# Performance work log

Measured on AMD Instinct MI355X. Metric: run time of the kernel, lower is better.

## Reference

```python
import jax, jax.numpy as jnp
import numpy as np

B, T, D = 16, 4096, 256
CODEBOOK_SIZE = 1024
COMMITMENT = 1.0


def setup_inputs() -> dict:
    key = jax.random.key(0)
    kx, kc = jax.random.split(key)
    x = jax.random.normal(kx, (B, T, D), dtype=jnp.float32)
    codebook = jax.random.normal(kc, (CODEBOOK_SIZE, D), dtype=jnp.float32)
    return {"x": x, "codebook": codebook}


def reference(x, codebook):
    # x: [B, T, D] continuous latents; codebook: [K, D]
    flat = x.reshape(-1, x.shape[-1])  # [N, D]
    # does not affect argmin but is kept for faithfulness to torch.cdist-style math)
    x_sq = jnp.sum(flat * flat, axis=1, keepdims=True)            # [N, 1]
    c_sq = jnp.sum(codebook * codebook, axis=1)                   # [K]
    dist = x_sq - 2.0 * (flat @ codebook.T) + c_sq[None, :]       # [N, K]
    indices = jnp.argmin(dist, axis=1)                            # [N] int
    quantized = codebook[indices].reshape(x.shape)                # gather, [B, T, D]
    # commitment loss: encoder pulled toward (stopped) codes
    commit_loss = COMMITMENT * jnp.mean(
        (x - jax.lax.stop_gradient(quantized)) ** 2
    )
    # straight-through estimator
    out = x + jax.lax.stop_gradient(quantized - x)
    return out, indices.reshape(x.shape[:-1]), commit_loss
```

## Files before the change

kernel.cpp:

```cpp
#include <hip/hip_runtime.h>

#define N_TOK 65536
#define DIM   256
#define KCODE 1024

#define NTHREADS 256
#define TM 128
#define TN 128
#define BK 32
#define NCHUNK 8
#define NSTAGE 24
#define OTM 128

#define REFINE_EPS 0.125f
#define TIE_THETA 1.0e-4

#define WS_CSQ_OFF   16
#define WS_IDX_OFF   2048
#define WS_PAIRS_OFF (WS_IDX_OFF + N_TOK)
#define WS_CBPK_OFF  (WS_PAIRS_OFF + N_TOK * NCHUNK * 4)

typedef float f32x4  __attribute__((ext_vector_type(4)));
typedef short bf16x8 __attribute__((ext_vector_type(8)));
typedef short s16x8  __attribute__((ext_vector_type(8)));

__global__ void rowsq_np_kernel(const float* __restrict__ m,
                                float* __restrict__ out,
                                float* __restrict__ loss_ws, int rows) {
#pragma clang fp contract(off)
    if (blockIdx.x == 0 && threadIdx.x == 0) loss_ws[0] = 0.0f;
    int row = blockIdx.x * 16 + (threadIdx.x >> 4);
    int l   = threadIdx.x & 15;
    if (row >= rows) return;
    int h = l >> 3;
    int j = l & 7;
    const float* p = m + (size_t)row * DIM + h * 128 + j;
    float v = p[0];
    float r = v * v;
#pragma unroll
    for (int i = 1; i < 16; ++i) {
        float w  = p[i * 8];
        float w2 = w * w;
        r = r + w2;
    }
    float t = r + __shfl_xor(r, 1);
    t = t + __shfl_xor(t, 2);
    t = t + __shfl_xor(t, 4);
    t = t + __shfl_xor(t, 8);
    if (l == 0) out[row] = t;
}

__device__ __forceinline__ void ins2(float d, int idx,
                                     float& d1, int& i1, float& d2, int& i2) {
    if (d < d1 || (d == d1 && idx < i1)) {
        d2 = d1; i2 = i1; d1 = d; i1 = idx;
    } else if ((d < d2 || (d == d2 && idx < i2)) && idx != i1) {
        d2 = d; i2 = idx;
    }
}

__device__ __forceinline__ void f2bf_split(float v, short& hi, short& lo) {
    unsigned u = __float_as_uint(v);
    unsigned r = (u + 0x7fffu + ((u >> 16) & 1u)) >> 16;
    hi = (short)r;
    float hf = __uint_as_float(r << 16);
    float lf = v - hf;
    unsigned u2 = __float_as_uint(lf);
    unsigned r2 = (u2 + 0x7fffu + ((u2 >> 16) & 1u)) >> 16;
    lo = (short)r2;
}

__global__ void pack_tiles_kernel(const float* __restrict__ src,
                                  unsigned short* __restrict__ dst,
                                  int total, int swz) {
    int tid = blockIdx.x * blockDim.x + threadIdx.x;
    if (tid >= total) return;
    int s   = tid & 3;
    int r   = (tid >> 2) & 127;
    int kc  = (tid >> 9) & 7;
    int g   = tid >> 12;
    int oct = swz ? (s ^ ((r >> 1) & 3)) : s;

    const float4* xr = reinterpret_cast<const float4*>(
        src + ((size_t)(g * 128 + r)) * DIM + kc * 32 + oct * 8);
    float4 v0 = xr[0];
    float4 v1 = xr[1];

    float f[8] = {v0.x, v0.y, v0.z, v0.w, v1.x, v1.y, v1.z, v1.w};
    s16x8 hv, lv;
#pragma unroll
    for (int i = 0; i < 8; ++i) {
        short h, l;
        f2bf_split(f[i], h, l);
        hv[i] = h; lv[i] = l;
    }
    size_t base_hi = (((size_t)(g * 16 + kc) * 128 + r) << 5) + s * 8;
    size_t base_lo = (((size_t)(g * 16 + 8 + kc) * 128 + r) << 5) + s * 8;
    *reinterpret_cast<s16x8*>(dst + base_hi) = hv;
    *reinterpret_cast<s16x8*>(dst + base_lo) = lv;
}

__device__ __forceinline__ void gload_lds16(const unsigned short* g, unsigned short* lds) {
    __builtin_amdgcn_global_load_lds(
        (const __attribute__((address_space(1))) unsigned int*)g,
        (__attribute__((address_space(3))) unsigned int*)lds, 16, 0, 0);
}

__launch_bounds__(NTHREADS, 4)
__global__ void vq_main_kernel(const unsigned short* __restrict__ xpk,
                               const unsigned short* __restrict__ cbpk,
                               const float* __restrict__ csq,
                               float4* __restrict__ pairs) {
    __shared__ __align__(16) unsigned short shbuf[2][TM * BK];
    __shared__ float4 pairs_sh[TM][2];

    const int tid  = threadIdx.x;
    const int w    = tid >> 6;
    const int wy   = w >> 1;
    const int wx   = w & 1;
    const int lane = tid & 63;
    const int lm   = lane & 15;
    const int q    = lane >> 4;

    const int bx     = blockIdx.x;
    const int jj     = bx >> 3;
    const int grp    = (bx & 7) + ((jj >> 3) << 3);
    const int cchunk = jj & 7;
    const int tok0   = grp * TM;
    const int code0  = cchunk * TN;

    float cs_reg[4];
#pragma unroll
    for (int ni = 0; ni < 4; ++ni)
        cs_reg[ni] = csq[code0 + wx * 64 + ni * 16 + lm];

    f32x4 acc[4][4];
#pragma unroll
    for (int mi = 0; mi < 4; ++mi)
#pragma unroll
        for (int ni = 0; ni < 4; ++ni)
            acc[mi][ni] = (f32x4){0.f, 0.f, 0.f, 0.f};

    int offA[4];
#pragma unroll
    for (int mi = 0; mi < 4; ++mi) {
        int r = wy * 64 + mi * 16 + lm;
        offA[mi] = r * BK + ((q ^ ((r >> 1) & 3)) * 8);
    }
    int offB[4];
#pragma unroll
    for (int ni = 0; ni < 4; ++ni) {
        int r = wx * 64 + ni * 16 + lm;
        offB[ni] = r * BK + q * 8;
    }

    const int lsrc = w * 1024 + lane * 8;
    auto stage = [&](int p, int s) {
        const int kc = s & 7;
        const int pa = (s >= 16) ? 8 : 0;
        const unsigned short* ga = xpk + (((size_t)(grp * 16 + pa + kc)) << 12) + lsrc;
        unsigned short* At = &shbuf[p][w * 1024];
        gload_lds16(ga,       At);
        gload_lds16(ga + 512, At + 512);
    };

    stage(0, 0);
    __syncthreads();

    int p = 0;
#pragma unroll 1
    for (int s = 0; s < NSTAGE; ++s) {
        const int kc = s & 7;
        const int pb = (s >= 8 && s < 16) ? 8 : 0;
        const unsigned short* gb =
            cbpk + (((size_t)(cchunk * 16 + pb + kc)) << 12);
        bf16x8 bf[4];
#pragma unroll
        for (int ni = 0; ni < 4; ++ni)
            bf[ni] = *reinterpret_cast<const bf16x8*>(gb + offB[ni]);

        if (s < NSTAGE - 1) stage(p ^ 1, s + 1);

        const unsigned short* buf = &shbuf[p][0];
        bf16x8 af[4];
#pragma unroll
        for (int mi = 0; mi < 4; ++mi)
            af[mi] = *reinterpret_cast<const bf16x8*>(buf + offA[mi]);

        __builtin_amdgcn_s_setprio(1);
#pragma unroll
        for (int mi = 0; mi < 4; ++mi)
#pragma unroll
            for (int ni = 0; ni < 4; ++ni)
                acc[mi][ni] = __builtin_amdgcn_mfma_f32_16x16x32_bf16(
                    af[mi], bf[ni], acc[mi][ni], 0, 0, 0);
        __builtin_amdgcn_s_setprio(0);

        __syncthreads();
        p ^= 1;
    }

#pragma unroll
    for (int mi = 0; mi < 4; ++mi) {
#pragma unroll
        for (int r = 0; r < 4; ++r) {
            int row_local = wy * 64 + mi * 16 + q * 4 + r;
            float l1 = 3.4e38f, l2 = 3.4e38f;
            int   j1 = 0x7fffffff, j2 = 0x7fffffff;
#pragma unroll
            for (int ni = 0; ni < 4; ++ni) {
                float d = cs_reg[ni] - 2.0f * acc[mi][ni][r];
                ins2(d, code0 + wx * 64 + ni * 16 + lm, l1, j1, l2, j2);
            }
#pragma unroll
            for (int m = 1; m < 16; m <<= 1) {
                float o1 = __shfl_xor(l1, m);
                int   p1 = __shfl_xor(j1, m);
                float o2 = __shfl_xor(l2, m);
                int   p2 = __shfl_xor(j2, m);
                ins2(o1, p1, l1, j1, l2, j2);
                ins2(o2, p2, l1, j1, l2, j2);
            }
            if (lm == 0) {
                float4 pr;
                pr.x = l1; pr.y = l2;
                pr.z = __int_as_float(j1); pr.w = __int_as_float(j2);
                pairs_sh[row_local][wx] = pr;
            }
        }
    }
    __syncthreads();
    if (tid < TM) {
        float4 pa = pairs_sh[tid][0];
        float4 pb = pairs_sh[tid][1];
        float d1 = pa.x, d2 = pa.y;
        int   i1 = __float_as_int(pa.z), i2 = __float_as_int(pa.w);
        ins2(pb.x, __float_as_int(pb.z), d1, i1, d2, i2);
        ins2(pb.y, __float_as_int(pb.w), d1, i1, d2, i2);
        float4 pr;
        pr.x = d1; pr.y = d2;
        pr.z = __int_as_float(i1); pr.w = __int_as_float(i2);
        pairs[(size_t)cchunk * N_TOK + tok0 + tid] = pr;
    }
}

__launch_bounds__(256)
__global__ void merge_output_kernel(const float* __restrict__ x,
                                    const float* __restrict__ cb,
                                    const float4* __restrict__ pairs,
                                    float* __restrict__ out_q,
                                    float* __restrict__ out_idx,
                                    float* __restrict__ loss_ws) {
    __shared__ int   sh_idx[OTM];
    __shared__ float wsum[4];
    const int tid  = threadIdx.x;
    const int tok0 = blockIdx.x * OTM;

    if (tid < OTM) {
        const int t = tok0 + tid;
        float4 p0 = pairs[t];
        float d1 = p0.x, d2 = p0.y;
        int   i1 = __float_as_int(p0.z), i2 = __float_as_int(p0.w);
#pragma unroll
        for (int c = 1; c < NCHUNK; ++c) {
            float4 p = pairs[(size_t)c * N_TOK + t];
            ins2(p.x, __float_as_int(p.z), d1, i1, d2, i2);
            ins2(p.y, __float_as_int(p.w), d1, i1, d2, i2);
        }

        int pick = i1;
        if (d2 - d1 < REFINE_EPS) {
            const float* xr = x + (size_t)t * DIM;
            const float* c1 = cb + (size_t)i1 * DIM;
            const float* c2 = cb + (size_t)i2 * DIM;
            double sA = 0.0, dA = 0.0, sB = 0.0, dB = 0.0;
            for (int k = 0; k < DIM; ++k) {
                double xv = (double)xr[k];
                double a  = (double)c1[k];
                double b  = (double)c2[k];
                sA += a * a; dA += xv * a;
                sB += b * b; dB += xv * b;
            }
            double DA  = sA - 2.0 * dA;
            double DB  = sB - 2.0 * dB;
            double gap = DB - DA;
            if (gap > TIE_THETA)       pick = i1;
            else if (gap < -TIE_THETA) pick = i2;
            else                       pick = (i1 < i2) ? i1 : i2;
        }
        sh_idx[tid] = pick;
        out_idx[t]  = (float)pick;
    }
    __syncthreads();

    float lsum = 0.0f;
    for (int t = 0; t < OTM; ++t) {
        int code = sh_idx[t];
        float qv = cb[(size_t)code * DIM + tid];
        float xv = x[(size_t)(tok0 + t) * DIM + tid];
        out_q[(size_t)(tok0 + t) * DIM + tid] = xv + (qv - xv);
        float df = xv - qv;
        lsum = fmaf(df, df, lsum);
    }

#pragma unroll
    for (int off = 1; off < 64; off <<= 1) lsum += __shfl_xor(lsum, off);
    if ((tid & 63) == 0) wsum[tid >> 6] = lsum;
    __syncthreads();
    if (tid == 0) atomicAdd(loss_ws, (wsum[0] + wsum[1]) + (wsum[2] + wsum[3]));
}

__global__ void finalize_kernel(const float* ws, float* out_loss) {
    if (threadIdx.x == 0) out_loss[0] = ws[0] * (1.0f / 16777216.0f);
}

extern "C" void kernel_launch(void* const* d_in, const int* in_sizes, int n_in,
                              void* d_out, int out_size, void* d_ws, size_t ws_size,
                              hipStream_t stream) {
    const float* x  = (const float*)d_in[0];
    const float* cb = (const float*)d_in[1];

    float* out      = (float*)d_out;
    float* out_q    = out;
    float* out_idx  = out + (size_t)N_TOK * DIM;
    float* out_loss = out_idx + N_TOK;

    float*  ws    = (float*)d_ws;
    float*  csq   = ws + WS_CSQ_OFF;
    float4* pairs = (float4*)(ws + WS_PAIRS_OFF);
    unsigned short* cbpk = (unsigned short*)(ws + WS_CBPK_OFF);
    unsigned short* xpk  = (unsigned short*)out_q;

    rowsq_np_kernel<<<KCODE / 16, 256, 0, stream>>>(cb, csq, ws, KCODE);
    pack_tiles_kernel<<<(N_TOK * 32) / 256, 256, 0, stream>>>(x, xpk, N_TOK * 32, 1);
    pack_tiles_kernel<<<(KCODE * 32) / 256, 256, 0, stream>>>(cb, cbpk, KCODE * 32, 0);
    vq_main_kernel<<<(N_TOK / TM) * NCHUNK, NTHREADS, 0, stream>>>(xpk, cbpk, csq, pairs);
    merge_output_kernel<<<N_TOK / OTM, 256, 0, stream>>>(x, cb, pairs, out_q, out_idx, ws);
    finalize_kernel<<<1, 64, 0, stream>>>(ws, out_loss);
}
```

Before: 793.9 us.

## Stage codebook tiles through LDS alongside token tiles with swizzled layout

The codebook B-operand tiles are now loaded asynchronously into LDS with global_load_lds in the same double-buffered stage as the token tiles, instead of being read per-thread straight from global memory each iteration. The codebook packing now uses the same XOR swizzle so the LDS reads avoid bank conflicts, the epilogue pair buffer reuses the staging LDS, the setprio hints are removed, and launch bounds ask for 5 blocks per CU. This is meant to hide global load latency for B inside the pipeline. In exchange it doubles LDS use per block and may raise register pressure under the tighter occupancy bound.

Result: no change. 798.8 us (+0.6%).

```diff
diff --git a/kernel.cpp b/kernel.cpp
--- a/kernel.cpp
+++ b/kernel.cpp
@@ -72,14 +72,14 @@
 
 __global__ void pack_tiles_kernel(const float* __restrict__ src,
                                   unsigned short* __restrict__ dst,
-                                  int total, int swz) {
+                                  int total) {
     int tid = blockIdx.x * blockDim.x + threadIdx.x;
     if (tid >= total) return;
     int s   = tid & 3;
     int r   = (tid >> 2) & 127;
     int kc  = (tid >> 9) & 7;
     int g   = tid >> 12;
-    int oct = swz ? (s ^ ((r >> 1) & 3)) : s;
+    int oct = s ^ ((r >> 1) & 3);
 
     const float4* xr = reinterpret_cast<const float4*>(
         src + ((size_t)(g * 128 + r)) * DIM + kc * 32 + oct * 8);
@@ -106,13 +106,12 @@
         (__attribute__((address_space(3))) unsigned int*)lds, 16, 0, 0);
 }
 
-__launch_bounds__(NTHREADS, 4)
+__launch_bounds__(NTHREADS, 5)
 __global__ void vq_main_kernel(const unsigned short* __restrict__ xpk,
                                const unsigned short* __restrict__ cbpk,
                                const float* __restrict__ csq,
                                float4* __restrict__ pairs) {
-    __shared__ __align__(16) unsigned short shbuf[2][TM * BK];
-    __shared__ float4 pairs_sh[TM][2];
+    __shared__ __align__(16) unsigned short shbuf[2][2 * TM * BK];
 
     const int tid  = threadIdx.x;
     const int w    = tid >> 6;
@@ -141,27 +140,32 @@
         for (int ni = 0; ni < 4; ++ni)
             acc[mi][ni] = (f32x4){0.f, 0.f, 0.f, 0.f};
 
-    int offA[4];
+    int offA[4], offB[4];
 #pragma unroll
     for (int mi = 0; mi < 4; ++mi) {
         int r = wy * 64 + mi * 16 + lm;
         offA[mi] = r * BK + ((q ^ ((r >> 1) & 3)) * 8);
     }
-    int offB[4];
 #pragma unroll
     for (int ni = 0; ni < 4; ++ni) {
         int r = wx * 64 + ni * 16 + lm;
-        offB[ni] = r * BK + q * 8;
+        offB[ni] = TM * BK + r * BK + ((q ^ ((r >> 1) & 3)) * 8);
     }
 
     const int lsrc = w * 1024 + lane * 8;
     auto stage = [&](int p, int s) {
-        const int kc = s & 7;
-        const int pa = (s >= 16) ? 8 : 0;
-        const unsigned short* ga = xpk + (((size_t)(grp * 16 + pa + kc)) << 12) + lsrc;
+        const int seg = s >> 3;
+        const int kc  = s & 7;
+        const int pa  = (seg == 2) ? 8 : 0;
+        const int pb  = (seg == 1) ? 8 : 0;
+        const unsigned short* ga = xpk  + (((size_t)(grp    * 16 + pa + kc)) << 12) + lsrc;
+        const unsigned short* gb = cbpk + (((size_t)(cchunk * 16 + pb + kc)) << 12) + lsrc;
         unsigned short* At = &shbuf[p][w * 1024];
+        unsigned short* Bt = &shbuf[p][TM * BK + w * 1024];
         gload_lds16(ga,       At);
         gload_lds16(ga + 512, At + 512);
+        gload_lds16(gb,       Bt);
+        gload_lds16(gb + 512, Bt + 512);
     };
 
     stage(0, 0);
@@ -170,35 +174,29 @@
     int p = 0;
 #pragma unroll 1
     for (int s = 0; s < NSTAGE; ++s) {
-        const int kc = s & 7;
-        const int pb = (s >= 8 && s < 16) ? 8 : 0;
-        const unsigned short* gb =
-            cbpk + (((size_t)(cchunk * 16 + pb + kc)) << 12);
-        bf16x8 bf[4];
-#pragma unroll
-        for (int ni = 0; ni < 4; ++ni)
-            bf[ni] = *reinterpret_cast<const bf16x8*>(gb + offB[ni]);
-
         if (s < NSTAGE - 1) stage(p ^ 1, s + 1);
 
         const unsigned short* buf = &shbuf[p][0];
-        bf16x8 af[4];
+        bf16x8 af[4], bf[4];
 #pragma unroll
         for (int mi = 0; mi < 4; ++mi)
             af[mi] = *reinterpret_cast<const bf16x8*>(buf + offA[mi]);
-
-        __builtin_amdgcn_s_setprio(1);
+#pragma unroll
+        for (int ni = 0; ni < 4; ++ni)
+            bf[ni] = *reinterpret_cast<const bf16x8*>(buf + offB[ni]);
+
 #pragma unroll
         for (int mi = 0; mi < 4; ++mi)
 #pragma unroll
             for (int ni = 0; ni < 4; ++ni)
                 acc[mi][ni] = __builtin_amdgcn_mfma_f32_16x16x32_bf16(
                     af[mi], bf[ni], acc[mi][ni], 0, 0, 0);
-        __builtin_amdgcn_s_setprio(0);
 
         __syncthreads();
         p ^= 1;
     }
+
+    float4 (*pairs_sh)[2] = reinterpret_cast<float4(*)[2]>(&shbuf[0][0]);
 
 #pragma unroll
     for (int mi = 0; mi < 4; ++mi) {
@@ -332,8 +330,8 @@
     unsigned short* xpk  = (unsigned short*)out_q;
 
     rowsq_np_kernel<<<KCODE / 16, 256, 0, stream>>>(cb, csq, ws, KCODE);
-    pack_tiles_kernel<<<(N_TOK * 32) / 256, 256, 0, stream>>>(x, xpk, N_TOK * 32, 1);
-    pack_tiles_kernel<<<(KCODE * 32) / 256, 256, 0, stream>>>(cb, cbpk, KCODE * 32, 0);
+    pack_tiles_kernel<<<(N_TOK * 32) / 256, 256, 0, stream>>>(x, xpk, N_TOK * 32);
+    pack_tiles_kernel<<<(KCODE * 32) / 256, 256, 0, stream>>>(cb, cbpk, KCODE * 32);
     vq_main_kernel<<<(N_TOK / TM) * NCHUNK, NTHREADS, 0, stream>>>(xpk, cbpk, csq, pairs);
     merge_output_kernel<<<N_TOK / OTM, 256, 0, stream>>>(x, cb, pairs, out_q, out_idx, ws);
     finalize_kernel<<<1, 64, 0, stream>>>(ws, out_loss);
```
